# Kernel optimization log

Measured on AMD Instinct MI355X. Metric: run time of the kernel, lower is better.

The kernel has to match this reference:

```python
import jax, jax.numpy as jnp
import numpy as np

N, E, F, H, G, C = 50000, 800000, 128, 64, 512, 10
RATIO = 0.5  # forward arg `ratio` baked as constant


def seg_mean(msgs, idx, n):
    s = jax.ops.segment_sum(msgs, idx, num_segments=n)
    cnt = jax.ops.segment_sum(jnp.ones(idx.shape[0], msgs.dtype), idx, num_segments=n)
    return s / jnp.maximum(cnt, 1.0)[:, None]


def sage(x, src, dst, Wl, bl, Wr, ew=None):
    # PyG SAGEConv: lin_l(mean_{j->i} msg_j) + lin_r(x_i); weighted variant scales messages
    m = x[src] if ew is None else x[src] * ew[:, None]
    agg = seg_mean(m, dst, x.shape[0])
    return agg @ Wl + bl + x @ Wr


def topk_mask(scores, seg, num_graphs, ratio):
    # per-graph (segment) top-k edge selection: keep ceil(ratio*edges_in_graph) highest scores
    e = scores.shape[0]
    counts = jax.ops.segment_sum(jnp.ones(e, jnp.float32), seg, num_segments=num_graphs)
    order = jnp.lexsort((-scores, seg))  # sort by segment, then score descending
    seg_sorted = seg[order]
    starts = jnp.concatenate([jnp.zeros(1, jnp.float32), jnp.cumsum(counts)[:-1]])
    rank = jnp.arange(e, dtype=jnp.float32) - starts[seg_sorted]
    k = jnp.ceil(ratio * counts)
    sel = (rank < k[seg_sorted]).astype(scores.dtype)
    return jnp.zeros(e, scores.dtype).at[order].set(sel)


def setup_inputs():
    key = jax.random.key(0)
    ks = jax.random.split(key, 16)
    w = lambda k, shape, fan: (jax.random.normal(k, shape, jnp.float32) / np.sqrt(fan))
    return {
        'x': jax.random.normal(ks[0], (N, F), jnp.float32),
        'edge_index': jax.random.randint(ks[1], (2, E), 0, N, jnp.int32),
        'batch': jnp.sort(jax.random.randint(ks[2], (N,), 0, G, jnp.int32)),
        'W1l': w(ks[3], (F, H), F), 'b1l': jnp.zeros(H, jnp.float32), 'W1r': w(ks[4], (F, H), F),
        'W2l': w(ks[5], (H, H), H), 'b2l': jnp.zeros(H, jnp.float32), 'W2r': w(ks[6], (H, H), H),
        'W3l': w(ks[7], (H, H), H), 'b3l': jnp.zeros(H, jnp.float32), 'W3r': w(ks[8], (H, H), H),
        'Wlin1': w(ks[9], (H, H), H), 'blin1': jnp.zeros(H, jnp.float32),
        'Wlin2': w(ks[10], (H, C), H), 'blin2': jnp.zeros(C, jnp.float32),
    }


def reference(x, edge_index, batch, W1l, b1l, W1r, W2l, b2l, W2r, W3l, b3l, W3r, Wlin1, blin1, Wlin2, blin2):
    src, dst = edge_index[0], edge_index[1]
    h = jax.nn.relu(sage(x, src, dst, W1l, b1l, W1r))
    edge_scores = jnp.sum(h[src] * h[dst], axis=-1)  # [E]
    seg = batch[src]  # graph id per edge (sections)
    sampled = topk_mask(edge_scores, seg, G, RATIO)
    ew = edge_scores * sampled
    h = jax.nn.relu(sage(h, src, dst, W2l, b2l, W2r, ew))
    h = jax.nn.relu(sage(h, src, dst, W3l, b3l, W3r, ew))
    pooled = seg_mean(h, batch, G)  # global_mean_pool
    z = jax.nn.relu(pooled @ Wlin1 + blin1)
    z = z @ Wlin2 + blin2  # dropout inactive in eval
    return jax.nn.log_softmax(z, axis=-1), sampled
```

## Files before the change

### kernel.cpp

```cpp
#include <hip/hip_runtime.h>
#include <hip/hip_bf16.h>
#include <math.h>

static constexpr int N = 50000;
static constexpr int E = 800000;
static constexpr int F = 128;
static constexpr int H = 64;
static constexpr int G = 512;
static constexpr int C = 10;
static constexpr int CAP = 256;

static inline int cdiv(long a, int b) { return (int)((a + b - 1) / b); }

__device__ __forceinline__ float uinv_score(unsigned u) {
  return (u & 0x80000000u) ? __uint_as_float(u & 0x7fffffffu) : __uint_as_float(~u);
}

__global__ void k_deg_goff(const int* __restrict__ dst, const int* __restrict__ batch,
                           int* __restrict__ deg, int* __restrict__ goff) {
  for (int i = blockIdx.x * 256 + threadIdx.x; i < N; i += gridDim.x * 256) {
    int b = batch[i];
    if (i == 0) {
      for (int g = 0; g <= b; ++g) goff[g] = 0;
    } else {
      int p = batch[i - 1];
      for (int g = p + 1; g <= b; ++g) goff[g] = i;
    }
    if (i == N - 1) {
      for (int g = b + 1; g <= G; ++g) goff[g] = N;
    }
  }
  for (int e = blockIdx.x * 256 + threadIdx.x; e < E; e += gridDim.x * 256)
    atomicAdd(&deg[dst[e]], 1);
}

__global__ void k_scan_a(const int* __restrict__ cnt, int* __restrict__ off,
                         int* __restrict__ bsum, int n) {
  __shared__ int wsum[16];
  int tid = threadIdx.x, lane = tid & 63, wv = tid >> 6;
  int idx = blockIdx.x * 4096 + tid * 4;
  int v0 = (idx + 0 < n) ? cnt[idx + 0] : 0;
  int v1 = (idx + 1 < n) ? cnt[idx + 1] : 0;
  int v2 = (idx + 2 < n) ? cnt[idx + 2] : 0;
  int v3 = (idx + 3 < n) ? cnt[idx + 3] : 0;
  int local = v0 + v1 + v2 + v3;
  int inc = local;
  for (int d = 1; d < 64; d <<= 1) {
    int t = __shfl_up(inc, d);
    if (lane >= d) inc += t;
  }
  if (lane == 63) wsum[wv] = inc;
  __syncthreads();
  if (tid < 16) {
    int t = wsum[tid];
    for (int d = 1; d < 16; d <<= 1) {
      int u = __shfl_up(t, d);
      if (tid >= d) t += u;
    }
    wsum[tid] = t;
  }
  __syncthreads();
  int woff = (wv > 0) ? wsum[wv - 1] : 0;
  int excl = woff + inc - local;
  if (idx + 0 < n) off[idx + 0] = excl;
  if (idx + 1 < n) off[idx + 1] = excl + v0;
  if (idx + 2 < n) off[idx + 2] = excl + v0 + v1;
  if (idx + 3 < n) off[idx + 3] = excl + v0 + v1 + v2;
  if (tid == 0) bsum[blockIdx.x] = wsum[15];
}

__global__ void k_scan_b(int* __restrict__ bsum, int nb) {
  int lane = threadIdx.x;
  int v = (lane < nb) ? bsum[lane] : 0;
  int inc = v;
  for (int d = 1; d < 64; d <<= 1) {
    int t = __shfl_up(inc, d);
    if (lane >= d) inc += t;
  }
  if (lane < nb) bsum[lane] = inc - v;
  if (lane == nb) bsum[nb] = inc;
}

__global__ void k_scan_c(int* __restrict__ off, int* __restrict__ cursor,
                         const int* __restrict__ bsum, int n, int nb) {
  int i = blockIdx.x * 256 + threadIdx.x;
  if (i < n) {
    int v = off[i] + bsum[i >> 12];
    off[i] = v;
    cursor[i] = v;
  } else if (i == n) {
    off[n] = bsum[nb];
  }
}

__global__ void k_fill_csr(const int* __restrict__ src, const int* __restrict__ dst,
                           int* __restrict__ cursor, int2* __restrict__ csr,
                           int* __restrict__ einv, int lo, int hi) {
  int e = blockIdx.x * 256 + threadIdx.x;
  if (e >= E) return;
  int d = dst[e];
  if (d < lo || d >= hi) return;
  int slot = atomicAdd(&cursor[d], 1);
  csr[slot] = make_int2(src[e], e);
  einv[e] = slot;
}

template <int K>
__global__ void k_gemm2(const float* __restrict__ in, const float* __restrict__ Wl,
                        const float* __restrict__ Wr, const float* __restrict__ b,
                        float* __restrict__ y, float* __restrict__ r) {
  __shared__ float sx[16][K];
  int lane = threadIdx.x, ty = threadIdx.y;
  int tid = ty * 64 + lane;
  int row0 = blockIdx.x * 16;
  const float4* gsrc = (const float4*)(in + (size_t)row0 * K);
  float4* sdst = (float4*)(&sx[0][0]);
#pragma unroll
  for (int i = tid; i < 16 * K / 4; i += 256) sdst[i] = gsrc[i];
  __syncthreads();
  float al[4], ar[4];
  float bias = b[lane];
#pragma unroll
  for (int j = 0; j < 4; ++j) { al[j] = 0.f; ar[j] = bias; }
#pragma unroll 4
  for (int f = 0; f < K; ++f) {
    float wl = Wl[f * H + lane];
    float wr = Wr[f * H + lane];
#pragma unroll
    for (int j = 0; j < 4; ++j) {
      float xv = sx[ty * 4 + j][f];
      al[j] += xv * wl;
      ar[j] += xv * wr;
    }
  }
#pragma unroll
  for (int j = 0; j < 4; ++j) {
    int row = row0 + ty * 4 + j;
    y[(size_t)row * H + lane] = al[j];
    r[(size_t)row * H + lane] = ar[j];
  }
}

template <int K>
__global__ void k_gemm2h(const float* __restrict__ in, const float* __restrict__ Wl,
                         const float* __restrict__ Wr, const float* __restrict__ b,
                         __hip_bfloat16* __restrict__ y, float* __restrict__ r) {
  __shared__ float sx[16][K];
  int lane = threadIdx.x, ty = threadIdx.y;
  int tid = ty * 64 + lane;
  int row0 = blockIdx.x * 16;
  const float4* gsrc = (const float4*)(in + (size_t)row0 * K);
  float4* sdst = (float4*)(&sx[0][0]);
#pragma unroll
  for (int i = tid; i < 16 * K / 4; i += 256) sdst[i] = gsrc[i];
  __syncthreads();
  float al[4], ar[4];
  float bias = b[lane];
#pragma unroll
  for (int j = 0; j < 4; ++j) { al[j] = 0.f; ar[j] = bias; }
#pragma unroll 4
  for (int f = 0; f < K; ++f) {
    float wl = Wl[f * H + lane];
    float wr = Wr[f * H + lane];
#pragma unroll
    for (int j = 0; j < 4; ++j) {
      float xv = sx[ty * 4 + j][f];
      al[j] += xv * wl;
      ar[j] += xv * wr;
    }
  }
#pragma unroll
  for (int j = 0; j < 4; ++j) {
    int row = row0 + ty * 4 + j;
    y[(size_t)row * H + lane] = __float2bfloat16(al[j]);
    r[(size_t)row * H + lane] = ar[j];
  }
}

__global__ void k_agg1(const float* __restrict__ y, const float* __restrict__ r,
                       const int2* __restrict__ csr, const int* __restrict__ off,
                       float* __restrict__ out) {
  int node = blockIdx.x * 8 + threadIdx.y;
  int lane = threadIdx.x;
  int q = lane >> 3, c = lane & 7;
  int s0 = off[node], s1 = off[node + 1];
  float4 a0 = make_float4(0.f, 0.f, 0.f, 0.f);
  float4 a1 = make_float4(0.f, 0.f, 0.f, 0.f);
  int i = s0 + q;
  for (; i + 8 < s1; i += 16) {
    int2 se0 = csr[i];
    int2 se1 = csr[i + 8];
    const float4* p0 = (const float4*)(y + (size_t)se0.x * H);
    const float4* p1 = (const float4*)(y + (size_t)se1.x * H);
    float4 u0 = p0[c], v0 = p0[c + 8];
    float4 u1 = p1[c], v1 = p1[c + 8];
    a0.x += u0.x + u1.x; a0.y += u0.y + u1.y; a0.z += u0.z + u1.z; a0.w += u0.w + u1.w;
    a1.x += v0.x + v1.x; a1.y += v0.y + v1.y; a1.z += v0.z + v1.z; a1.w += v0.w + v1.w;
  }
  for (; i < s1; i += 8) {
    int2 se = csr[i];
    const float4* p = (const float4*)(y + (size_t)se.x * H);
    float4 u = p[c], v = p[c + 8];
    a0.x += u.x; a0.y += u.y; a0.z += u.z; a0.w += u.w;
    a1.x += v.x; a1.y += v.y; a1.z += v.z; a1.w += v.w;
  }
#pragma unroll
  for (int d = 8; d < 64; d <<= 1) {
    a0.x += __shfl_xor(a0.x, d); a0.y += __shfl_xor(a0.y, d);
    a0.z += __shfl_xor(a0.z, d); a0.w += __shfl_xor(a0.w, d);
    a1.x += __shfl_xor(a1.x, d); a1.y += __shfl_xor(a1.y, d);
    a1.z += __shfl_xor(a1.z, d); a1.w += __shfl_xor(a1.w, d);
  }
  if (q == 0) {
    float inv = 1.f / fmaxf((float)(s1 - s0), 1.f);
    const float4* rp = (const float4*)(r + (size_t)node * H);
    float4 r0 = rp[c], r1 = rp[c + 8];
    float4 o0, o1;
    o0.x = fmaxf(a0.x * inv + r0.x, 0.f); o0.y = fmaxf(a0.y * inv + r0.y, 0.f);
    o0.z = fmaxf(a0.z * inv + r0.z, 0.f); o0.w = fmaxf(a0.w * inv + r0.w, 0.f);
    o1.x = fmaxf(a1.x * inv + r1.x, 0.f); o1.y = fmaxf(a1.y * inv + r1.y, 0.f);
    o1.z = fmaxf(a1.z * inv + r1.z, 0.f); o1.w = fmaxf(a1.w * inv + r1.w, 0.f);
    float4* op = (float4*)(out + (size_t)node * H);
    op[c] = o0; op[c + 8] = o1;
  }
}

__global__ void k_compact(const unsigned char* __restrict__ sel,
                          const int2* __restrict__ csr, const float* __restrict__ ewc,
                          const int* __restrict__ off, int2* __restrict__ csr2,
                          int* __restrict__ cnt2) {
  int node = blockIdx.x * 8 + threadIdx.y;
  int lane = threadIdx.x;
  int s0 = off[node], s1 = off[node + 1];
  unsigned long long lt = ((unsigned long long)1 << lane) - 1;
  int cum = 0;
  for (int i0 = s0; i0 < s1; i0 += 64) {
    int i = i0 + lane;
    bool f = (i < s1) && sel[i];
    unsigned long long m = __ballot(f);
    if (f) {
      int rank = __popcll(m & lt);
      int2 se = csr[i];
      csr2[s0 + cum + rank] = make_int2(se.x, __float_as_int(ewc[i]));
    }
    cum += __popcll(m);
  }
  if (lane == 0) cnt2[node] = cum;
}

__global__ void k_agg_w(const __hip_bfloat16* __restrict__ y, const float* __restrict__ r,
                        const int2* __restrict__ csr2, const int* __restrict__ cnt2,
                        const int* __restrict__ off, float* __restrict__ out) {
  int node = blockIdx.x * 8 + threadIdx.y;
  int lane = threadIdx.x;
  int q = lane >> 3, c = lane & 7;
  int b0 = off[node], cn = cnt2[node];
  float a[8] = {0.f, 0.f, 0.f, 0.f, 0.f, 0.f, 0.f, 0.f};
  for (int j = q; j < cn; j += 8) {
    int2 sw = csr2[b0 + j];
    float w = __int_as_float(sw.y);
    uint4 pk = ((const uint4*)((const unsigned short*)y + (size_t)sw.x * H))[c];
    a[0] += w * __uint_as_float(pk.x << 16); a[1] += w * __uint_as_float(pk.x & 0xffff0000u);
    a[2] += w * __uint_as_float(pk.y << 16); a[3] += w * __uint_as_float(pk.y & 0xffff0000u);
    a[4] += w * __uint_as_float(pk.z << 16); a[5] += w * __uint_as_float(pk.z & 0xffff0000u);
    a[6] += w * __uint_as_float(pk.w << 16); a[7] += w * __uint_as_float(pk.w & 0xffff0000u);
  }
#pragma unroll
  for (int d = 8; d < 64; d <<= 1) {
#pragma unroll
    for (int j = 0; j < 8; ++j) a[j] += __shfl_xor(a[j], d);
  }
  if (q == 0) {
    int degn = off[node + 1] - off[node];
    float inv = 1.f / fmaxf((float)degn, 1.f);
    const float4* rp = (const float4*)(r + (size_t)node * H);
    float4 r0 = rp[2 * c], r1 = rp[2 * c + 1];
    float4 o0, o1;
    o0.x = fmaxf(a[0] * inv + r0.x, 0.f); o0.y = fmaxf(a[1] * inv + r0.y, 0.f);
    o0.z = fmaxf(a[2] * inv + r0.z, 0.f); o0.w = fmaxf(a[3] * inv + r0.w, 0.f);
    o1.x = fmaxf(a[4] * inv + r1.x, 0.f); o1.y = fmaxf(a[5] * inv + r1.y, 0.f);
    o1.z = fmaxf(a[6] * inv + r1.z, 0.f); o1.w = fmaxf(a[7] * inv + r1.w, 0.f);
    float4* op = (float4*)(out + (size_t)node * H);
    op[2 * c] = o0; op[2 * c + 1] = o1;
  }
}

__global__ void k_score_csr(const float* __restrict__ h1, const int2* __restrict__ csr,
                            const int* __restrict__ off, const int* __restrict__ batch,
                            unsigned* __restrict__ scoreu_csr,
                            unsigned short* __restrict__ seg_csr, int* __restrict__ hist) {
  int node = blockIdx.x * 8 + threadIdx.y;
  int lane = threadIdx.x;
  int q = lane >> 4, c = lane & 15;
  int s0 = off[node], s1 = off[node + 1];
  float4 hn = ((const float4*)(h1 + (size_t)node * H))[c];
  int i = s0 + q;
  for (; i + 4 < s1; i += 8) {
    int2 se0 = csr[i];
    int2 se1 = csr[i + 4];
    float4 hs0 = ((const float4*)(h1 + (size_t)se0.x * H))[c];
    float4 hs1 = ((const float4*)(h1 + (size_t)se1.x * H))[c];
    float p0 = hn.x * hs0.x + hn.y * hs0.y + hn.z * hs0.z + hn.w * hs0.w;
    float p1 = hn.x * hs1.x + hn.y * hs1.y + hn.z * hs1.z + hn.w * hs1.w;
    p0 += __shfl_xor(p0, 1); p1 += __shfl_xor(p1, 1);
    p0 += __shfl_xor(p0, 2); p1 += __shfl_xor(p1, 2);
    p0 += __shfl_xor(p0, 4); p1 += __shfl_xor(p1, 4);
    p0 += __shfl_xor(p0, 8); p1 += __shfl_xor(p1, 8);
    if (c == 0) {
      int g0 = batch[se0.x], g1 = batch[se1.x];
      unsigned u0 = __float_as_uint(p0); u0 = (u0 & 0x80000000u) ? ~u0 : (u0 | 0x80000000u);
      unsigned u1 = __float_as_uint(p1); u1 = (u1 & 0x80000000u) ? ~u1 : (u1 | 0x80000000u);
      scoreu_csr[i] = u0; scoreu_csr[i + 4] = u1;
      seg_csr[i] = (unsigned short)g0; seg_csr[i + 4] = (unsigned short)g1;
      atomicAdd(&hist[g0 * 256 + (int)(u0 >> 24)], 1);
      atomicAdd(&hist[g1 * 256 + (int)(u1 >> 24)], 1);
    }
  }
  for (; i < s1; i += 4) {
    int2 se = csr[i];
    float4 hs = ((const float4*)(h1 + (size_t)se.x * H))[c];
    float p = hn.x * hs.x + hn.y * hs.y + hn.z * hs.z + hn.w * hs.w;
    p += __shfl_xor(p, 1);
    p += __shfl_xor(p, 2);
    p += __shfl_xor(p, 4);
    p += __shfl_xor(p, 8);
    if (c == 0) {
      int g = batch[se.x];
      unsigned u = __float_as_uint(p);
      u = (u & 0x80000000u) ? ~u : (u | 0x80000000u);
      scoreu_csr[i] = u;
      seg_csr[i] = (unsigned short)g;
      atomicAdd(&hist[g * 256 + (int)(u >> 24)], 1);
    }
  }
}

__global__ void k_hist(const unsigned* __restrict__ scoreu, const unsigned short* __restrict__ seg,
                       const unsigned* __restrict__ prefix, int* __restrict__ hist, int pass) {
  int e = blockIdx.x * 256 + threadIdx.x;
  if (e >= E) return;
  unsigned u = scoreu[e];
  int g = (int)seg[e];
  int predshift = 32 - 8 * pass;
  if ((u >> predshift) == (prefix[g] >> predshift))
    atomicAdd(&hist[g * 256 + (int)((u >> (24 - 8 * pass)) & 0xFFu)], 1);
}

__global__ void k_scan(int* __restrict__ hist, unsigned* __restrict__ prefix,
                       int* __restrict__ krem, int pass) {
  int g = blockIdx.x;
  int lane = threadIdx.x;
  int4* row = (int4*)(hist + (size_t)g * 256);
  int4 v = row[lane];
  int vj[4] = {v.x, v.y, v.z, v.w};
  int s = v.x + v.y + v.z + v.w;
  int inc = s;
  for (int d = 1; d < 64; d <<= 1) {
    int t = __shfl_up(inc, d);
    if (lane >= d) inc += t;
  }
  int T = __shfl(inc, 63);
  int k = (pass == 0) ? ((T + 1) >> 1) : krem[g];
  int excl = inc - s;
  int pre[4] = {excl, excl + vj[0], excl + vj[0] + vj[1], excl + vj[0] + vj[1] + vj[2]};
  int bsel_l = -1, newk_l = 0;
  if (k > 0) {
    for (int j = 3; j >= 0; --j) {
      int suf = T - pre[j];
      if (suf >= k) { bsel_l = 4 * lane + j; newk_l = k - (suf - vj[j]); break; }
    }
  }
  unsigned long long mask = __ballot(bsel_l >= 0);
  int bsel = 255, newk = 0;
  if (k > 0 && mask) {
    int hi = 63 - __builtin_clzll(mask);
    bsel = __shfl(bsel_l, hi);
    newk = __shfl(newk_l, hi);
  }
  if (lane == 0) {
    unsigned base = (pass == 0) ? 0u : prefix[g];
    prefix[g] = base | ((unsigned)bsel << (24 - 8 * pass));
    krem[g] = newk;
  }
  row[lane] = make_int4(0, 0, 0, 0);
}

__global__ void k_select(const unsigned* __restrict__ scoreu_csr,
                         const unsigned short* __restrict__ seg_csr,
                         const unsigned* __restrict__ thresh,
                         int* __restrict__ eqcnt, int* __restrict__ eqlist,
                         unsigned char* __restrict__ sel_csr, float* __restrict__ ew_csr) {
  int s = blockIdx.x * 256 + threadIdx.x;
  if (s >= E) return;
  unsigned u = scoreu_csr[s];
  int g = (int)seg_csr[s];
  unsigned t = thresh[g];
  unsigned um = u & 0xffffff00u;
  float sel = 0.f;
  if (um > t) sel = 1.f;
  else if (um == t) {
    int slot = atomicAdd(&eqcnt[g], 1);
    if (slot < CAP) eqlist[g * CAP + slot] = s;
  }
  sel_csr[s] = (unsigned char)sel;
  ew_csr[s] = uinv_score(u) * sel;
}

__global__ void k_resolve(const int* __restrict__ krem, const int* __restrict__ eqcnt,
                          const int* __restrict__ eqlist, const int2* __restrict__ csr,
                          const unsigned* __restrict__ scoreu_csr,
                          unsigned char* __restrict__ sel_csr, float* __restrict__ ew_csr) {
  int g = blockIdx.x * 256 + threadIdx.x;
  if (g >= G) return;
  int c = eqcnt[g]; if (c > CAP) c = CAP;
  int r = krem[g];  if (r > c) r = c;
  const int* lst = eqlist + g * CAP;
  unsigned last_u = 0u; int last_e = -1; bool first = true;
  for (int i = 0; i < r; ++i) {
    unsigned bu = 0u; int be = -1, bs = -1;
    for (int j = 0; j < c; ++j) {
      int slot = lst[j];
      unsigned u = scoreu_csr[slot];
      int eid = csr[slot].y;
      bool after = first || (u < last_u) || (u == last_u && eid > last_e);
      if (after && (bs < 0 || u > bu || (u == bu && eid < be))) { bu = u; be = eid; bs = slot; }
    }
    if (bs < 0) break;
    sel_csr[bs] = 1;
    ew_csr[bs] = uinv_score(bu);
    last_u = bu; last_e = be; first = false;
  }
}

__global__ void k_sampled(const int* __restrict__ einv, const unsigned char* __restrict__ sel_csr,
                          float* __restrict__ sampled) {
  int e = (blockIdx.x * 256 + threadIdx.x) * 4;
  if (e >= E) return;
  int4 iv = *(const int4*)(einv + e);
  float4 o;
  o.x = (float)sel_csr[iv.x];
  o.y = (float)sel_csr[iv.y];
  o.z = (float)sel_csr[iv.z];
  o.w = (float)sel_csr[iv.w];
  *(float4*)(sampled + e) = o;
}

__global__ void k_poolhead(const float* __restrict__ h3, const int* __restrict__ goff,
                           const float* __restrict__ W1, const float* __restrict__ b1,
                           const float* __restrict__ W2, const float* __restrict__ b2,
                           float* __restrict__ outp) {
  int g = blockIdx.x;
  int h = threadIdx.x;
  int s0 = goff[g], s1 = goff[g + 1];
  float a = 0.f;
  for (int n = s0; n < s1; ++n) a += h3[(size_t)n * H + h];
  float inv = 1.f / fmaxf((float)(s1 - s0), 1.f);
  __shared__ float p[H], z1[H], z2[C];
  __shared__ float lse;
  p[h] = a * inv;
  __syncthreads();
  float acc = b1[h];
#pragma unroll 8
  for (int f = 0; f < H; ++f) acc += p[f] * W1[f * H + h];
  z1[h] = fmaxf(acc, 0.f);
  __syncthreads();
  if (h < C) {
    float a2 = b2[h];
#pragma unroll 8
    for (int f = 0; f < H; ++f) a2 += z1[f] * W2[f * C + h];
    z2[h] = a2;
  }
  __syncthreads();
  if (h == 0) {
    float m = z2[0];
    for (int c = 1; c < C; ++c) m = fmaxf(m, z2[c]);
    float s = 0.f;
    for (int c = 0; c < C; ++c) s += expf(z2[c] - m);
    lse = m + logf(s);
  }
  __syncthreads();
  if (h < C) outp[(size_t)g * C + h] = z2[h] - lse;
}

extern "C" void kernel_launch(void* const* d_in, const int* in_sizes, int n_in,
                              void* d_out, int out_size, void* d_ws, size_t ws_size,
                              hipStream_t stream) {
  const float* x     = (const float*)d_in[0];
  const int*   ei    = (const int*)d_in[1];
  const int*   batch = (const int*)d_in[2];
  const float* W1l   = (const float*)d_in[3];
  const float* b1l   = (const float*)d_in[4];
  const float* W1r   = (const float*)d_in[5];
  const float* W2l   = (const float*)d_in[6];
  const float* b2l   = (const float*)d_in[7];
  const float* W2r   = (const float*)d_in[8];
  const float* W3l   = (const float*)d_in[9];
  const float* b3l   = (const float*)d_in[10];
  const float* W3r   = (const float*)d_in[11];
  const float* Wlin1 = (const float*)d_in[12];
  const float* blin1 = (const float*)d_in[13];
  const float* Wlin2 = (const float*)d_in[14];
  const float* blin2 = (const float*)d_in[15];

  const int* srcv = ei;
  const int* dstv = ei + E;

  float* out_ls   = (float*)d_out;
  float* out_samp = out_ls + G * C;

  char* w = (char*)d_ws;
  auto carve = [&](size_t bytes) { void* p = (void*)w; w += (bytes + 255) & ~(size_t)255; return p; };
  char* zbase   = w;
  int*      deg     = (int*)carve((size_t)N * 4);
  int*      eqcnt   = (int*)carve((size_t)G * 4);
  int*      hist    = (int*)carve((size_t)G * 256 * 4);
  size_t    zbytes  = (size_t)(w - zbase);
  float*    h1      = (float*)carve((size_t)N * H * 4);
  float*    h2      = (float*)carve((size_t)N * H * 4);
  float*    h3      = (float*)carve((size_t)N * H * 4);
  float*    yb      = (float*)carve((size_t)N * H * 4);
  float*    rb      = (float*)carve((size_t)N * H * 4);
  __hip_bfloat16* ybh = (__hip_bfloat16*)carve((size_t)N * H * 2);
  unsigned* scoreu_csr = (unsigned*)carve((size_t)E * 4);
  unsigned short* seg_csr = (unsigned short*)carve((size_t)E * 2);
  float*    ew_csr     = (float*)carve((size_t)E * 4);
  unsigned char* sel_csr = (unsigned char*)carve((size_t)E);
  int2*     csr     = (int2*)carve((size_t)E * 8);
  int*      einv    = (int*)carve((size_t)E * 4);
  int*      off     = (int*)carve((size_t)(N + 1) * 4);
  int*      cursor  = (int*)carve((size_t)N * 4);
  int*      cnt2    = (int*)carve((size_t)N * 4);
  int*      goff    = (int*)carve((size_t)(G + 1) * 4);
  unsigned* prefix  = (unsigned*)carve((size_t)G * 4);
  int*      krem    = (int*)carve((size_t)G * 4);
  int*      eqlist  = (int*)carve((size_t)G * CAP * 4);
  int*      bsum    = (int*)carve((size_t)16 * 4);
  int2*     csr2    = (int2*)carve((size_t)E * 8);

  hipMemsetAsync(zbase, 0, zbytes, stream);

  k_deg_goff<<<128, 256, 0, stream>>>(dstv, batch, deg, goff);
  int nb = cdiv(N, 4096);
  k_scan_a<<<nb, 1024, 0, stream>>>(deg, off, bsum, N);
  k_scan_b<<<1, 64, 0, stream>>>(bsum, nb);
  k_scan_c<<<cdiv(N + 1, 256), 256, 0, stream>>>(off, cursor, bsum, N, nb);
  k_fill_csr<<<cdiv(E, 256), 256, 0, stream>>>(srcv, dstv, cursor, csr, einv, 0, N / 2);
  k_fill_csr<<<cdiv(E, 256), 256, 0, stream>>>(srcv, dstv, cursor, csr, einv, N / 2, N);

  k_gemm2<F><<<N / 16, dim3(64, 4), 0, stream>>>(x, W1l, W1r, b1l, yb, rb);
  k_agg1<<<N / 8, dim3(64, 8), 0, stream>>>(yb, rb, csr, off, h1);

  k_score_csr<<<N / 8, dim3(64, 8), 0, stream>>>(h1, csr, off, batch,
                                                 scoreu_csr, seg_csr, hist);
  k_scan<<<G, 64, 0, stream>>>(hist, prefix, krem, 0);
  for (int p = 1; p <= 2; ++p) {
    k_hist<<<cdiv(E, 256), 256, 0, stream>>>(scoreu_csr, seg_csr, prefix, hist, p);
    k_scan<<<G, 64, 0, stream>>>(hist, prefix, krem, p);
  }
  k_select<<<cdiv(E, 256), 256, 0, stream>>>(scoreu_csr, seg_csr, prefix,
                                             eqcnt, eqlist, sel_csr, ew_csr);
  k_resolve<<<cdiv(G, 256), 256, 0, stream>>>(krem, eqcnt, eqlist, csr, scoreu_csr,
                                              sel_csr, ew_csr);
  k_sampled<<<cdiv(E / 4, 256), 256, 0, stream>>>(einv, sel_csr, out_samp);

  k_compact<<<N / 8, dim3(64, 8), 0, stream>>>(sel_csr, csr, ew_csr, off, csr2, cnt2);

  k_gemm2h<H><<<N / 16, dim3(64, 4), 0, stream>>>(h1, W2l, W2r, b2l, ybh, rb);
  k_agg_w<<<N / 8, dim3(64, 8), 0, stream>>>(ybh, rb, csr2, cnt2, off, h2);

  k_gemm2h<H><<<N / 16, dim3(64, 4), 0, stream>>>(h2, W3l, W3r, b3l, ybh, rb);
  k_agg_w<<<N / 8, dim3(64, 8), 0, stream>>>(ybh, rb, csr2, cnt2, off, h3);

  k_poolhead<<<G, 64, 0, stream>>>(h3, goff, Wlin1, blin1, Wlin2, blin2, out_ls);
}
```

Baseline: 499.2 us.

## Flatten edge scoring, cut radix passes, fuse scan kernels, parallelize pool head

Several changes land together. Edge scoring becomes flat over CSR slots, with a stored per-slot destination, so each wave handles 8 edges with independent gathers instead of looping per node. The top-k radix selection drops from three passes to two, selecting on a 16-bit prefix, and the hist and select kernels are vectorized to process four edges per thread. The small block-sum scan is folded into k_scan_c, the two fill_csr launches are merged into one grid, and pool-head pooling now uses 512 threads. Together these remove launches and improve memory parallelism. The trade-off is more ties routed to the eqlist resolve path, which risks overflowing CAP.

```diff
diff --git a/kernel.cpp b/kernel.cpp
--- a/kernel.cpp
+++ b/kernel.cpp
@@ -69,39 +69,45 @@
   if (tid == 0) bsum[blockIdx.x] = wsum[15];
 }
 
-__global__ void k_scan_b(int* __restrict__ bsum, int nb) {
-  int lane = threadIdx.x;
-  int v = (lane < nb) ? bsum[lane] : 0;
-  int inc = v;
-  for (int d = 1; d < 64; d <<= 1) {
-    int t = __shfl_up(inc, d);
-    if (lane >= d) inc += t;
-  }
-  if (lane < nb) bsum[lane] = inc - v;
-  if (lane == nb) bsum[nb] = inc;
-}
-
 __global__ void k_scan_c(int* __restrict__ off, int* __restrict__ cursor,
                          const int* __restrict__ bsum, int n, int nb) {
-  int i = blockIdx.x * 256 + threadIdx.x;
+  __shared__ int spre[34];
+  int tid = threadIdx.x;
+  if (tid < 32) {
+    int v = (tid < nb) ? bsum[tid] : 0;
+    int inc = v;
+    for (int d = 1; d < 32; d <<= 1) {
+      int t = __shfl_up(inc, d);
+      if (tid >= d) inc += t;
+    }
+    spre[tid] = inc - v;
+  }
+  __syncthreads();
+  int i = blockIdx.x * 256 + tid;
   if (i < n) {
-    int v = off[i] + bsum[i >> 12];
+    int v = off[i] + spre[i >> 12];
     off[i] = v;
     cursor[i] = v;
   } else if (i == n) {
-    off[n] = bsum[nb];
+    off[n] = spre[nb];
   }
 }
 
 __global__ void k_fill_csr(const int* __restrict__ src, const int* __restrict__ dst,
                            int* __restrict__ cursor, int2* __restrict__ csr,
-                           int* __restrict__ einv, int lo, int hi) {
-  int e = blockIdx.x * 256 + threadIdx.x;
+                           int* __restrict__ dsts, int* __restrict__ einv) {
+  int half = gridDim.x >> 1;
+  int win = (blockIdx.x < half) ? 0 : 1;
+  int blk = (win == 0) ? blockIdx.x : (blockIdx.x - half);
+  int e = blk * 256 + threadIdx.x;
   if (e >= E) return;
   int d = dst[e];
+  int lo = win ? (N / 2) : 0;
+  int hi = win ? N : (N / 2);
   if (d < lo || d >= hi) return;
   int slot = atomicAdd(&cursor[d], 1);
   csr[slot] = make_int2(src[e], e);
+  dsts[slot] = d;
   einv[e] = slot;
 }
 
@@ -286,64 +292,57 @@
 }
 
 __global__ void k_score_csr(const float* __restrict__ h1, const int2* __restrict__ csr,
-                            const int* __restrict__ off, const int* __restrict__ batch,
+                            const int* __restrict__ dsts, const int* __restrict__ batch,
                             unsigned* __restrict__ scoreu_csr,
                             unsigned short* __restrict__ seg_csr, int* __restrict__ hist) {
-  int node = blockIdx.x * 8 + threadIdx.y;
   int lane = threadIdx.x;
   int q = lane >> 4, c = lane & 15;
-  int s0 = off[node], s1 = off[node + 1];
-  float4 hn = ((const float4*)(h1 + (size_t)node * H))[c];
-  int i = s0 + q;
-  for (; i + 4 < s1; i += 8) {
-    int2 se0 = csr[i];
-    int2 se1 = csr[i + 4];
-    float4 hs0 = ((const float4*)(h1 + (size_t)se0.x * H))[c];
-    float4 hs1 = ((const float4*)(h1 + (size_t)se1.x * H))[c];
-    float p0 = hn.x * hs0.x + hn.y * hs0.y + hn.z * hs0.z + hn.w * hs0.w;
-    float p1 = hn.x * hs1.x + hn.y * hs1.y + hn.z * hs1.z + hn.w * hs1.w;
-    p0 += __shfl_xor(p0, 1); p1 += __shfl_xor(p1, 1);
-    p0 += __shfl_xor(p0, 2); p1 += __shfl_xor(p1, 2);
-    p0 += __shfl_xor(p0, 4); p1 += __shfl_xor(p1, 4);
-    p0 += __shfl_xor(p0, 8); p1 += __shfl_xor(p1, 8);
-    if (c == 0) {
-      int g0 = batch[se0.x], g1 = batch[se1.x];
-      unsigned u0 = __float_as_uint(p0); u0 = (u0 & 0x80000000u) ? ~u0 : (u0 | 0x80000000u);
-      unsigned u1 = __float_as_uint(p1); u1 = (u1 & 0x80000000u) ? ~u1 : (u1 | 0x80000000u);
-      scoreu_csr[i] = u0; scoreu_csr[i + 4] = u1;
-      seg_csr[i] = (unsigned short)g0; seg_csr[i + 4] = (unsigned short)g1;
-      atomicAdd(&hist[g0 * 256 + (int)(u0 >> 24)], 1);
-      atomicAdd(&hist[g1 * 256 + (int)(u1 >> 24)], 1);
-    }
-  }
-  for (; i < s1; i += 4) {
-    int2 se = csr[i];
-    float4 hs = ((const float4*)(h1 + (size_t)se.x * H))[c];
-    float p = hn.x * hs.x + hn.y * hs.y + hn.z * hs.z + hn.w * hs.w;
-    p += __shfl_xor(p, 1);
-    p += __shfl_xor(p, 2);
-    p += __shfl_xor(p, 4);
-    p += __shfl_xor(p, 8);
-    if (c == 0) {
-      int g = batch[se.x];
-      unsigned u = __float_as_uint(p);
+  int s = (blockIdx.x * 8 + threadIdx.y) * 32 + q * 8;
+  int sr[8], dd[8];
+#pragma unroll
+  for (int j = 0; j < 8; ++j) { sr[j] = csr[s + j].x; dd[j] = dsts[s + j]; }
+  float4 xr[8], yr[8];
+#pragma unroll
+  for (int j = 0; j < 8; ++j) xr[j] = ((const float4*)(h1 + (size_t)sr[j] * H))[c];
+#pragma unroll
+  for (int j = 0; j < 8; ++j) yr[j] = ((const float4*)(h1 + (size_t)dd[j] * H))[c];
+  float p[8];
+#pragma unroll
+  for (int j = 0; j < 8; ++j)
+    p[j] = yr[j].x * xr[j].x + yr[j].y * xr[j].y + yr[j].z * xr[j].z + yr[j].w * xr[j].w;
+#pragma unroll
+  for (int d = 1; d < 16; d <<= 1) {
+#pragma unroll
+    for (int j = 0; j < 8; ++j) p[j] += __shfl_xor(p[j], d);
+  }
+  if (c == 0) {
+#pragma unroll
+    for (int j = 0; j < 8; ++j) {
+      int g = batch[sr[j]];
+      unsigned u = __float_as_uint(p[j]);
       u = (u & 0x80000000u) ? ~u : (u | 0x80000000u);
-      scoreu_csr[i] = u;
-      seg_csr[i] = (unsigned short)g;
+      scoreu_csr[s + j] = u;
+      seg_csr[s + j] = (unsigned short)g;
       atomicAdd(&hist[g * 256 + (int)(u >> 24)], 1);
     }
   }
 }
 
-__global__ void k_hist(const unsigned* __restrict__ scoreu, const unsigned short* __restrict__ seg,
-                       const unsigned* __restrict__ prefix, int* __restrict__ hist, int pass) {
-  int e = blockIdx.x * 256 + threadIdx.x;
+__global__ void k_hist1(const unsigned* __restrict__ scoreu, const unsigned short* __restrict__ seg,
+                        const unsigned* __restrict__ prefix, int* __restrict__ hist) {
+  int e = (blockIdx.x * 256 + threadIdx.x) * 4;
   if (e >= E) return;
-  unsigned u = scoreu[e];
-  int g = (int)seg[e];
-  int predshift = 32 - 8 * pass;
-  if ((u >> predshift) == (prefix[g] >> predshift))
-    atomicAdd(&hist[g * 256 + (int)((u >> (24 - 8 * pass)) & 0xFFu)], 1);
+  uint4 u4 = *(const uint4*)(scoreu + e);
+  ushort4 s4 = *(const ushort4*)(seg + e);
+  unsigned uu[4] = {u4.x, u4.y, u4.z, u4.w};
+  int gg[4] = {(int)s4.x, (int)s4.y, (int)s4.z, (int)s4.w};
+#pragma unroll
+  for (int j = 0; j < 4; ++j) {
+    unsigned u = uu[j];
+    int g = gg[j];
+    if ((u >> 24) == (prefix[g] >> 24))
+      atomicAdd(&hist[g * 256 + (int)((u >> 16) & 0xFFu)], 1);
+  }
 }
 
 __global__ void k_scan(int* __restrict__ hist, unsigned* __restrict__ prefix,
@@ -390,20 +389,31 @@
                          const unsigned* __restrict__ thresh,
                          int* __restrict__ eqcnt, int* __restrict__ eqlist,
                          unsigned char* __restrict__ sel_csr, float* __restrict__ ew_csr) {
-  int s = blockIdx.x * 256 + threadIdx.x;
+  int s = (blockIdx.x * 256 + threadIdx.x) * 4;
   if (s >= E) return;
-  unsigned u = scoreu_csr[s];
-  int g = (int)seg_csr[s];
-  unsigned t = thresh[g];
-  unsigned um = u & 0xffffff00u;
-  float sel = 0.f;
-  if (um > t) sel = 1.f;
-  else if (um == t) {
-    int slot = atomicAdd(&eqcnt[g], 1);
-    if (slot < CAP) eqlist[g * CAP + slot] = s;
-  }
-  sel_csr[s] = (unsigned char)sel;
-  ew_csr[s] = uinv_score(u) * sel;
+  uint4 u4 = *(const uint4*)(scoreu_csr + s);
+  ushort4 g4 = *(const ushort4*)(seg_csr + s);
+  unsigned uu[4] = {u4.x, u4.y, u4.z, u4.w};
+  int gg[4] = {(int)g4.x, (int)g4.y, (int)g4.z, (int)g4.w};
+  float ew[4];
+  unsigned char sl[4];
+#pragma unroll
+  for (int j = 0; j < 4; ++j) {
+    unsigned u = uu[j];
+    int g = gg[j];
+    unsigned t = thresh[g];
+    unsigned um = u & 0xffff0000u;
+    float sel = 0.f;
+    if (um > t) sel = 1.f;
+    else if (um == t) {
+      int slot = atomicAdd(&eqcnt[g], 1);
+      if (slot < CAP) eqlist[g * CAP + slot] = s + j;
+    }
+    sl[j] = (unsigned char)sel;
+    ew[j] = uinv_score(u) * sel;
+  }
+  *(uchar4*)(sel_csr + s) = make_uchar4(sl[0], sl[1], sl[2], sl[3]);
+  *(float4*)(ew_csr + s) = make_float4(ew[0], ew[1], ew[2], ew[3]);
 }
 
 __global__ void k_resolve(const int* __restrict__ krem, const int* __restrict__ eqcnt,
@@ -450,28 +460,38 @@
                            const float* __restrict__ W2, const float* __restrict__ b2,
                            float* __restrict__ outp) {
   int g = blockIdx.x;
-  int h = threadIdx.x;
+  int tid = threadIdx.x;
+  int h = tid & 63, j = tid >> 6;
   int s0 = goff[g], s1 = goff[g + 1];
   float a = 0.f;
-  for (int n = s0; n < s1; ++n) a += h3[(size_t)n * H + h];
-  float inv = 1.f / fmaxf((float)(s1 - s0), 1.f);
+  for (int n = s0 + j; n < s1; n += 8) a += h3[(size_t)n * H + h];
+  __shared__ float sp[8][H];
   __shared__ float p[H], z1[H], z2[C];
   __shared__ float lse;
-  p[h] = a * inv;
-  __syncthreads();
-  float acc = b1[h];
+  sp[j][h] = a;
+  __syncthreads();
+  if (j == 0) {
+    float s = sp[0][h] + sp[1][h] + sp[2][h] + sp[3][h]
+            + sp[4][h] + sp[5][h] + sp[6][h] + sp[7][h];
+    float inv = 1.f / fmaxf((float)(s1 - s0), 1.f);
+    p[h] = s * inv;
+  }
+  __syncthreads();
+  if (j == 0) {
+    float acc = b1[h];
 #pragma unroll 8
-  for (int f = 0; f < H; ++f) acc += p[f] * W1[f * H + h];
-  z1[h] = fmaxf(acc, 0.f);
-  __syncthreads();
-  if (h < C) {
-    float a2 = b2[h];
+    for (int f = 0; f < H; ++f) acc += p[f] * W1[f * H + h];
+    z1[h] = fmaxf(acc, 0.f);
+  }
+  __syncthreads();
+  if (tid < C) {
+    float a2 = b2[tid];
 #pragma unroll 8
-    for (int f = 0; f < H; ++f) a2 += z1[f] * W2[f * C + h];
-    z2[h] = a2;
-  }
-  __syncthreads();
-  if (h == 0) {
+    for (int f = 0; f < H; ++f) a2 += z1[f] * W2[f * C + tid];
+    z2[tid] = a2;
+  }
+  __syncthreads();
+  if (tid == 0) {
     float m = z2[0];
     for (int c = 1; c < C; ++c) m = fmaxf(m, z2[c]);
     float s = 0.f;
@@ -479,7 +499,7 @@
     lse = m + logf(s);
   }
   __syncthreads();
-  if (h < C) outp[(size_t)g * C + h] = z2[h] - lse;
+  if (tid < C) outp[(size_t)g * C + tid] = z2[tid] - lse;
 }
 
 extern "C" void kernel_launch(void* const* d_in, const int* in_sizes, int n_in,
@@ -526,6 +546,7 @@
   float*    ew_csr     = (float*)carve((size_t)E * 4);
   unsigned char* sel_csr = (unsigned char*)carve((size_t)E);
   int2*     csr     = (int2*)carve((size_t)E * 8);
+  int*      dsts    = (int*)carve((size_t)E * 4);
   int*      einv    = (int*)carve((size_t)E * 4);
   int*      off     = (int*)carve((size_t)(N + 1) * 4);
   int*      cursor  = (int*)carve((size_t)N * 4);
@@ -539,26 +560,22 @@
 
   hipMemsetAsync(zbase, 0, zbytes, stream);
 
-  k_deg_goff<<<128, 256, 0, stream>>>(dstv, batch, deg, goff);
+  k_deg_goff<<<256, 256, 0, stream>>>(dstv, batch, deg, goff);
   int nb = cdiv(N, 4096);
   k_scan_a<<<nb, 1024, 0, stream>>>(deg, off, bsum, N);
-  k_scan_b<<<1, 64, 0, stream>>>(bsum, nb);
   k_scan_c<<<cdiv(N + 1, 256), 256, 0, stream>>>(off, cursor, bsum, N, nb);
-  k_fill_csr<<<cdiv(E, 256), 256, 0, stream>>>(srcv, dstv, cursor, csr, einv, 0, N / 2);
-  k_fill_csr<<<cdiv(E, 256), 256, 0, stream>>>(srcv, dstv, cursor, csr, einv, N / 2, N);
+  k_fill_csr<<<2 * cdiv(E, 256), 256, 0, stream>>>(srcv, dstv, cursor, csr, dsts, einv);
 
   k_gemm2<F><<<N / 16, dim3(64, 4), 0, stream>>>(x, W1l, W1r, b1l, yb, rb);
   k_agg1<<<N / 8, dim3(64, 8), 0, stream>>>(yb, rb, csr, off, h1);
 
-  k_score_csr<<<N / 8, dim3(64, 8), 0, stream>>>(h1, csr, off, batch,
-                                                 scoreu_csr, seg_csr, hist);
+  k_score_csr<<<E / 256, dim3(64, 8), 0, stream>>>(h1, csr, dsts, batch,
+                                                   scoreu_csr, seg_csr, hist);
   k_scan<<<G, 64, 0, stream>>>(hist, prefix, krem, 0);
-  for (int p = 1; p <= 2; ++p) {
-    k_hist<<<cdiv(E, 256), 256, 0, stream>>>(scoreu_csr, seg_csr, prefix, hist, p);
-    k_scan<<<G, 64, 0, stream>>>(hist, prefix, krem, p);
-  }
-  k_select<<<cdiv(E, 256), 256, 0, stream>>>(scoreu_csr, seg_csr, prefix,
-                                             eqcnt, eqlist, sel_csr, ew_csr);
+  k_hist1<<<cdiv(E / 4, 256), 256, 0, stream>>>(scoreu_csr, seg_csr, prefix, hist);
+  k_scan<<<G, 64, 0, stream>>>(hist, prefix, krem, 1);
+  k_select<<<cdiv(E / 4, 256), 256, 0, stream>>>(scoreu_csr, seg_csr, prefix,
+                                                 eqcnt, eqlist, sel_csr, ew_csr);
   k_resolve<<<cdiv(G, 256), 256, 0, stream>>>(krem, eqcnt, eqlist, csr, scoreu_csr,
                                               sel_csr, ew_csr);
   k_sampled<<<cdiv(E / 4, 256), 256, 0, stream>>>(einv, sel_csr, out_samp);
@@ -571,5 +588,5 @@
   k_gemm2h<H><<<N / 16, dim3(64, 4), 0, stream>>>(h2, W3l, W3r, b3l, ybh, rb);
   k_agg_w<<<N / 8, dim3(64, 8), 0, stream>>>(ybh, rb, csr2, cnt2, off, h3);
 
-  k_poolhead<<<G, 64, 0, stream>>>(h3, goff, Wlin1, blin1, Wlin2, blin2, out_ls);
-}
+  k_poolhead<<<G, 512, 0, stream>>>(h3, goff, Wlin1, blin1, Wlin2, blin2, out_ls);
+}
```

After: 576.7 us. 1.16x slower.
